# Performance work log

Measured on AMD Instinct MI355X. Metric: run time of the kernel, lower is better.

## Reference

```python
import jax, jax.numpy as jnp
import numpy as np

F = 4        # number of factors
M = 256      # codebook size per factor
D = 8192     # hypervector dimension
B = 256      # batch of composite vectors to factorize
ITERS = 10   # resonator iterations


def setup_inputs() -> dict:
    key = jax.random.key(0)
    k1, k2 = jax.random.split(key, 2)
    # bipolar (+1/-1) codebooks, shape [F, M, D]
    cb = jnp.sign(jax.random.normal(k1, (F, M, D), dtype=jnp.float32))
    codebooks = jnp.where(cb == 0, 1.0, cb)
    # composite inputs: bind (elementwise product) of one random codevector per factor
    idx = jax.random.randint(k2, (B, F), 0, M)                       # [B, F]
    chosen = codebooks[jnp.arange(F)[None, :], idx]                  # [B, F, D]
    inp = jnp.prod(chosen, axis=1)                                   # [B, D]
    return {"input": inp, "codebooks": codebooks}


def _stage_concurrent(inp, est, codebooks):
    # est: [B, F, D]; codebooks: [F, M, D]; inp: [B, D]
    n = est.shape[1]
    # inv_others[:, f] = prod_{j != f} est[:, j]  (bipolar inverse == identity)
    inv_others = jnp.stack(
        [jnp.prod(jnp.concatenate([est[:, :f], est[:, f + 1:]], axis=1), axis=1)
         for f in range(n)], axis=1)                                  # [B, F, D]
    new_est = inp[:, None, :] * inv_others                            # bind -> [B, F, D]
    sim = jnp.einsum('bfd,fmd->bfm', new_est, codebooks)              # similarity
    # activation == 'NONE'
    out = jnp.einsum('bfm,fmd->bfd', sim, codebooks)                  # dot_similarity
    return jnp.sign(out)


def reference(input, codebooks):
    Bn = input.shape[0]
    # init estimates = multiset (sum) of each codebook, broadcast over batch
    init = jnp.broadcast_to(jnp.sum(codebooks, axis=1)[None], (Bn, F, D)).astype(input.dtype)

    def cond(state):
        _, k, done = state
        return jnp.logical_and(k < ITERS, jnp.logical_not(done))

    def body(state):
        est, k, _ = state
        new = _stage_concurrent(input, est, codebooks)
        return (new, k + 1, jnp.all(new == est))

    est, k, _ = jax.lax.while_loop(cond, body, (init, jnp.int32(0), jnp.array(False)))
    # cleanup: nearest codevector per factor (argmax similarity)
    sim = jnp.einsum('bfd,fmd->bfm', est, codebooks)
    outcome = jnp.argmax(sim, axis=-1)                                # [B, F] indices
    return outcome, k
```

## Files before the change

kernel.cpp:

```cpp
#include <hip/hip_runtime.h>

#define B_SZ 256
#define F_SZ 4
#define M_SZ 256
#define D_SZ 8192
#define NITER 10

typedef signed char i8;
typedef unsigned long long u64;
typedef signed char c16 __attribute__((ext_vector_type(16)));
typedef int v4i __attribute__((ext_vector_type(4)));

#define NBFM (B_SZ * F_SZ * M_SZ)

#define OFF_CB    ((size_t)0)
#define OFF_CBT   ((size_t)8  << 20)
#define OFF_IN8   ((size_t)16 << 20)
#define OFF_CBBT  ((size_t)18 << 20)
#define OFF_INB   ((size_t)19 << 20)
#define OFF_ESB   ((size_t)20 << 20)
#define OFF_EZB   ((size_t)21 << 20)
#define OFF_SIMX  ((size_t)22 << 20)
#define OFF_P1    ((size_t)23 << 20)
#define OFF_S32   ((size_t)48 << 20)
#define OFF_PDIG  (OFF_S32 + (size_t)F_SZ * D_SZ * 4)
#define OFF_CHG   (OFF_PDIG + (size_t)3 * F_SZ * D_SZ)


__global__ __launch_bounds__(256) void k_cvt_cb(const float* __restrict__ src,
                                                i8* __restrict__ cb, i8* __restrict__ cbt) {
  __shared__ i8 tile[32][33];
  const int bid = blockIdx.x;
  const int f = bid >> 11;
  const int rem = bid & 2047;
  const int m0 = (rem >> 8) << 5;
  const int d0 = (rem & 255) << 5;
  const int t = threadIdx.x;
  const int i = t >> 3, j = (t & 7) << 2;
  const float4 v = *(const float4*)(src + ((size_t)(f * M_SZ + m0 + i)) * D_SZ + d0 + j);
  char4 c;
  c.x = v.x > 0.f ? 1 : -1;
  c.y = v.y > 0.f ? 1 : -1;
  c.z = v.z > 0.f ? 1 : -1;
  c.w = v.w > 0.f ? 1 : -1;
  *(char4*)(cb + ((size_t)(f * M_SZ + m0 + i)) * D_SZ + d0 + j) = c;
  tile[i][j + 0] = c.x; tile[i][j + 1] = c.y; tile[i][j + 2] = c.z; tile[i][j + 3] = c.w;
  __syncthreads();
  const int dd = t >> 3, jm = (t & 7) << 2;
  char4 o;
  o.x = tile[jm + 0][dd]; o.y = tile[jm + 1][dd]; o.z = tile[jm + 2][dd]; o.w = tile[jm + 3][dd];
  *(char4*)(cbt + ((size_t)(f * D_SZ + d0 + dd)) * M_SZ + m0 + jm) = o;
}

__global__ __launch_bounds__(256) void k_cvt_in(const float* __restrict__ src, i8* __restrict__ dst) {
  const int idx = blockIdx.x * 256 + threadIdx.x;
  const float4 v = ((const float4*)src)[idx];
  char4 c;
  c.x = v.x > 0.f ? 1 : -1;
  c.y = v.y > 0.f ? 1 : -1;
  c.z = v.z > 0.f ? 1 : -1;
  c.w = v.w > 0.f ? 1 : -1;
  ((char4*)dst)[idx] = c;
}

__global__ __launch_bounds__(256) void k_pack_cb(const i8* __restrict__ cb, u64* __restrict__ cbbT) {
  const int id = blockIdx.x * 256 + threadIdx.x;
  const int f = id >> 15;
  const int rem = id & 32767;
  const int w = rem >> 8;
  const int m = rem & 255;
  const i8* src = cb + ((size_t)(f * M_SZ + m)) * D_SZ + w * 64;
  u64 r = 0;
  #pragma unroll
  for (int k = 0; k < 4; ++k) {
    c16 v = *(const c16*)(src + k * 16);
    u64 part = 0;
    #pragma unroll
    for (int j = 0; j < 16; ++j) part |= ((u64)(((unsigned char)v[j]) >> 7)) << j;
    r |= part << (k * 16);
  }
  cbbT[((size_t)(f * 128 + w)) * 256 + m] = r;
}

__global__ __launch_bounds__(256) void k_pack_in(const i8* __restrict__ in8, u64* __restrict__ inb) {
  const int id = blockIdx.x * 256 + threadIdx.x;
  const int b = id >> 7;
  const int w = id & 127;
  const i8* src = in8 + (size_t)b * D_SZ + w * 64;
  u64 r = 0;
  #pragma unroll
  for (int k = 0; k < 4; ++k) {
    c16 v = *(const c16*)(src + k * 16);
    u64 part = 0;
    #pragma unroll
    for (int j = 0; j < 16; ++j) part |= ((u64)(((unsigned char)v[j]) >> 7)) << j;
    r |= part << (k * 16);
  }
  inb[(size_t)b * 128 + w] = r;
}

__global__ __launch_bounds__(256) void k_S(const i8* __restrict__ cb, int* __restrict__ S) {
  const int id = blockIdx.x * 256 + threadIdx.x;
  const int f = id >> 13, d = id & 8191;
  const i8* p = cb + (size_t)f * M_SZ * D_SZ + d;
  int s = 0;
  for (int m = 0; m < M_SZ; ++m) s += p[(size_t)m * D_SZ];
  S[id] = s;
}

__global__ __launch_bounds__(256) void k_P(const int* __restrict__ S, i8* __restrict__ pdig) {
  const int d = blockIdx.x * 256 + threadIdx.x;
  const int s0 = S[d], s1 = S[D_SZ + d], s2 = S[2 * D_SZ + d], s3 = S[3 * D_SZ + d];
  int P[4];
  P[0] = s1 * s2 * s3;
  P[1] = s0 * s2 * s3;
  P[2] = s0 * s1 * s3;
  P[3] = s0 * s1 * s2;
  for (int f = 0; f < 4; ++f) {
    int x = P[f] >> 3;
    #pragma unroll
    for (int p = 0; p < 2; ++p) {
      const int y = x + 127;
      const int q = (y >= 0) ? (y / 255) : -((-y + 254) / 255);
      const int dg = x - q * 255;
      pdig[((size_t)(p * F_SZ + f)) * D_SZ + d] = (i8)dg;
      x = q;
    }
    pdig[((size_t)(2 * F_SZ + f)) * D_SZ + d] = (i8)x;
  }
}


__global__ __launch_bounds__(256) void ga2_kernel(
    const i8* __restrict__ in8, const i8* __restrict__ cb,
    const i8* __restrict__ pdig, int* __restrict__ p1)
{
  __shared__ __align__(16) i8 lA[64 * 48];
  __shared__ __align__(16) i8 lB[128 * 48];

  const int bid = blockIdx.x;
  const int s = bid & 7;
  const int r = bid >> 3;
  const int p = r % 3;
  const int q = r / 3;
  const int f = q & 3;
  const int ct = q >> 2;
  const int b0 = (ct >> 1) * 64;
  const int m0 = (ct & 1) * 128;
  const int ksteps = 32;
  const int kbase = s << 10;

  const int t = threadIdx.x;
  const int lane = t & 63;
  const int wv = t >> 6;
  const int wrow = (wv >> 1) * 32;
  const int wcol = (wv & 1) * 64;

  const int arow = t >> 1;
  const int aoff = (t & 1) * 16;
  const i8* pB  = cb   + ((size_t)(f * M_SZ + m0 + arow)) * D_SZ + aoff;
  const i8* pDg = pdig + ((size_t)(p * F_SZ + f)) * D_SZ + aoff;
  const i8* pIn = in8  + (size_t)(b0 + arow) * D_SZ + aoff;

  v4i acc[2][4];
  #pragma unroll
  for (int tr = 0; tr < 2; ++tr)
    #pragma unroll
    for (int tc = 0; tc < 4; ++tc) acc[tr][tc] = 0;

  c16 va = 0, vb = 0;
  {
    const int kk = kbase;
    vb = (*(const c16*)(pB + kk)) * (*(const c16*)(pDg + kk));
    if (t < 128) va = *(const c16*)(pIn + kk);
  }

  for (int j = 0; j < ksteps; ++j) {
    c16 sa = va, sb = vb;
    if (j + 1 < ksteps) {
      const int kk = kbase + (j + 1) * 32;
      vb = (*(const c16*)(pB + kk)) * (*(const c16*)(pDg + kk));
      if (t < 128) va = *(const c16*)(pIn + kk);
    }
    __syncthreads();
    if (t < 128) *(c16*)&lA[arow * 48 + aoff] = sa;
    *(c16*)&lB[arow * 48 + aoff] = sb;
    __syncthreads();

    const int rsel = lane & 15;
    const int kq = (lane >> 4) * 8;
    long af[2], bf[4];
    #pragma unroll
    for (int tr = 0; tr < 2; ++tr) af[tr] = *(const long*)&lA[(wrow + tr * 16 + rsel) * 48 + kq];
    #pragma unroll
    for (int tc = 0; tc < 4; ++tc) bf[tc] = *(const long*)&lB[(wcol + tc * 16 + rsel) * 48 + kq];
    #pragma unroll
    for (int tr = 0; tr < 2; ++tr)
      #pragma unroll
      for (int tc = 0; tc < 4; ++tc)
        acc[tr][tc] = __builtin_amdgcn_mfma_i32_16x16x32_i8(af[tr], bf[tc], acc[tr][tc], 0, 0, 0);
  }

  const int colb = lane & 15;
  const int rowq = (lane >> 4) * 4;
  const size_t obase = (size_t)(p * 8 + s) * NBFM;
  #pragma unroll
  for (int tr = 0; tr < 2; ++tr)
    #pragma unroll
    for (int tc = 0; tc < 4; ++tc)
      #pragma unroll
      for (int rr = 0; rr < 4; ++rr) {
        const int b = b0 + wrow + tr * 16 + rowq + rr;
        const int m = m0 + wcol + tc * 16 + colb;
        p1[obase + (((size_t)(b * F_SZ + f)) << 8) + m] = acc[tr][tc][rr];
      }
}

__global__ __launch_bounds__(256) void k_digits1(const int* __restrict__ p1, i8* __restrict__ simx) {
  const int idx = blockIdx.x * 256 + threadIdx.x;
  long long g[3];
  #pragma unroll
  for (int p = 0; p < 3; ++p) {
    long long gg = 0;
    #pragma unroll
    for (int s = 0; s < 8; ++s) gg += (long long)p1[(size_t)(p * 8 + s) * NBFM + idx];
    g[p] = gg;
  }
  const long long sim = g[0] + 255LL * g[1] + 65025LL * g[2];
  int x = (int)sim;
  const int r1 = (x + 128) >> 8;
  const int d0 = x - (r1 << 8);
  const int r2 = (r1 + 128) >> 8;
  const int d1 = r1 - (r2 << 8);
  const size_t bf = (size_t)(idx >> 8);
  const int m = idx & 255;
  simx[bf * 768 + m] = (i8)d0;
  simx[bf * 768 + 256 + m] = (i8)d1;
  simx[bf * 768 + 512 + m] = (i8)r2;
}


__global__ __launch_bounds__(256) void ga_bit(
    const u64* __restrict__ esb, const u64* __restrict__ ezb,
    const u64* __restrict__ inb, const u64* __restrict__ cbbT,
    i8* __restrict__ simx, const int* __restrict__ changed, int it)
{
  __shared__ u64 AL[128][4];
  __shared__ int C0[2];

  if (changed[it - 1] == 0) return;

  const int bid = blockIdx.x;
  const int f = bid & 3;
  const int b0 = (bid >> 2) * 2;
  const int t = threadIdx.x;
  if (t < 2) C0[t] = 0;
  __syncthreads();

  {
    const int r = t >> 7, w = t & 127;
    const int b = b0 + r;
    int ffs[3]; int c = 0;
    for (int ff = 0; ff < 4; ++ff) if (ff != f) ffs[c++] = ff;
    const size_t base = (size_t)b * 4 * 128;
    const u64 s = inb[(size_t)b * 128 + w]
      ^ esb[base + ffs[0] * 128 + w] ^ esb[base + ffs[1] * 128 + w] ^ esb[base + ffs[2] * 128 + w];
    const u64 nz = ~(ezb[base + ffs[0] * 128 + w] | ezb[base + ffs[1] * 128 + w] | ezb[base + ffs[2] * 128 + w]);
    AL[w][r * 2] = s;
    AL[w][r * 2 + 1] = nz;
    int pcv = (int)__popcll(nz);
    #pragma unroll
    for (int off = 32; off >= 1; off >>= 1) pcv += __shfl_down(pcv, off);
    if ((t & 63) == 0) atomicAdd(&C0[r], pcv);
  }
  __syncthreads();

  const int m = t;
  int a0 = 0, a1 = 0;
  const u64* pc = cbbT + (size_t)f * 128 * 256 + m;
  #pragma unroll 4
  for (int w = 0; w < 128; ++w) {
    const u64 cbw = pc[w * 256];
    const u64 s0 = AL[w][0], z0 = AL[w][1], s1 = AL[w][2], z1 = AL[w][3];
    a0 += (int)__popcll((s0 ^ cbw) & z0);
    a1 += (int)__popcll((s1 ^ cbw) & z1);
  }
  const int sim0 = C0[0] - 2 * a0;
  const int sim1 = C0[1] - 2 * a1;

  int d1 = (sim0 + 128) >> 8; int d0v = sim0 - (d1 << 8);
  const size_t bf0 = ((size_t)b0 * 4 + f) * 768;
  simx[bf0 + m] = (i8)d0v; simx[bf0 + 256 + m] = (i8)d1;
  d1 = (sim1 + 128) >> 8; d0v = sim1 - (d1 << 8);
  const size_t bf1 = ((size_t)(b0 + 1) * 4 + f) * 768;
  simx[bf1 + m] = (i8)d0v; simx[bf1 + 256 + m] = (i8)d1;
}


template<int NP, bool FIRST>
__global__ __launch_bounds__(256) void gb_kernel(
    const i8* __restrict__ simx, const i8* __restrict__ cbt,
    u64* __restrict__ esb, u64* __restrict__ ezb,
    const int* __restrict__ S32,
    int* __restrict__ changed, int it)
{
  __shared__ __align__(16) i8 lB[8 * 8 * 64 * 8];
  __shared__ int chgf;

  if (!FIRST) { if (changed[it - 1] == 0) return; }

  const int bid = blockIdx.x;
  const int f = bid & 3;
  const int ct = bid >> 2;
  const int b0 = (ct >> 6) * 64;
  const int d0 = (ct & 63) * 128;

  const int t = threadIdx.x;
  if (t == 0) chgf = 0;
  const int lane = t & 63;
  const int wv = t >> 6;
  const int wrow = (wv >> 1) * 32;
  const int wcol = (wv & 1) * 64;

  {
    const int c = t & 15;
    const int dr0 = t >> 4;
    const int ks = c >> 1;
    const int q0 = (c & 1) * 2;
    #pragma unroll
    for (int i = 0; i < 8; ++i) {
      const int dr = dr0 + i * 16;
      union { c16 v; u64 u[2]; } x;
      x.v = *(const c16*)(cbt + ((size_t)(f * D_SZ + d0 + dr)) * M_SZ + c * 16);
      const int tile = dr >> 4;
      const int col = dr & 15;
      *(u64*)&lB[((((ks * 8 + tile) * 4 + q0) * 16 + col)) * 8] = x.u[0];
      *(u64*)&lB[((((ks * 8 + tile) * 4 + q0 + 1) * 16 + col)) * 8] = x.u[1];
    }
  }
  __syncthreads();

  v4i acc[NP][2][4];
  #pragma unroll
  for (int pp = 0; pp < NP; ++pp)
    #pragma unroll
    for (int tr = 0; tr < 2; ++tr)
      #pragma unroll
      for (int tc = 0; tc < 4; ++tc) acc[pp][tr][tc] = 0;

  const int rsel = lane & 15;
  const int kq = (lane >> 4) * 8;
  const int tb = wcol >> 4;

  #pragma unroll
  for (int ks = 0; ks < 8; ++ks) {
    long bf[4];
    #pragma unroll
    for (int tc = 0; tc < 4; ++tc)
      bf[tc] = *(const long*)&lB[((ks * 8 + tb + tc) * 64 + lane) * 8];
    #pragma unroll
    for (int pp = 0; pp < NP; ++pp) {
      long af[2];
      #pragma unroll
      for (int tr = 0; tr < 2; ++tr) {
        const int row = b0 + wrow + tr * 16 + rsel;
        af[tr] = *(const long*)(simx + ((size_t)(row * 4 + f)) * 768 + pp * 256 + ks * 32 + kq);
      }
      #pragma unroll
      for (int tr = 0; tr < 2; ++tr)
        #pragma unroll
        for (int tc = 0; tc < 4; ++tc)
          acc[pp][tr][tc] = __builtin_amdgcn_mfma_i32_16x16x32_i8(af[tr], bf[tc], acc[pp][tr][tc], 0, 0, 0);
    }
  }

  bool chl = false;
  const int colb = lane & 15;

  #pragma unroll
  for (int tr = 0; tr < 2; ++tr) {
    unsigned long long bs[4][4], bz[4][4];
    #pragma unroll
    for (int rr = 0; rr < 4; ++rr)
      #pragma unroll
      for (int tc = 0; tc < 4; ++tc) {
        int o = acc[0][tr][tc][rr];
        if (NP > 1) o += acc[1][tr][tc][rr] * 256;
        if (NP > 2) o += acc[2][tr][tc][rr] * 65536;
        bs[rr][tc] = __ballot(o < 0);
        bz[rr][tc] = __ballot(o == 0);
        if (FIRST) {
          const int sg = (o > 0) - (o < 0);
          const int d = d0 + wcol + tc * 16 + colb;
          chl |= (sg != S32[f * D_SZ + d]);
        }
      }
    u64 ws = 0, wz = 0;
    #pragma unroll
    for (int rl = 0; rl < 16; ++rl) {
      const int g = rl >> 2, rr = rl & 3;
      u64 vs = 0, vz = 0;
      #pragma unroll
      for (int tc = 0; tc < 4; ++tc) {
        vs |= ((bs[rr][tc] >> (g * 16)) & 0xFFFFull) << (tc * 16);
        vz |= ((bz[rr][tc] >> (g * 16)) & 0xFFFFull) << (tc * 16);
      }
      if (lane == rl) { ws = vs; wz = vz; }
    }
    if (lane < 16) {
      const int row = b0 + wrow + tr * 16 + lane;
      const size_t wi = ((size_t)(row * 4 + f)) * 128 + ((d0 + wcol) >> 6);
      if (!FIRST) chl |= (ws != esb[wi]) | (wz != ezb[wi]);
      esb[wi] = ws;
      ezb[wi] = wz;
    }
  }
  if (chl) atomicOr(&chgf, 1);
  __syncthreads();
  if (t == 0 && chgf) atomicOr(&changed[it], 1);
}


__global__ __launch_bounds__(256) void k_final(
    const u64* __restrict__ esb, const u64* __restrict__ ezb,
    const u64* __restrict__ cbbT, const int* __restrict__ chg,
    int* __restrict__ out)
{
  __shared__ u64 AL[128][4];
  __shared__ int C0[2];
  __shared__ long long red0[256], red1[256];

  const int bid = blockIdx.x;
  const int f = bid & 3;
  const int b0 = (bid >> 2) * 2;
  const int t = threadIdx.x;
  if (t < 2) C0[t] = 0;
  __syncthreads();

  {
    const int r = t >> 7, w = t & 127;
    const int b = b0 + r;
    const size_t a = ((size_t)b * 4 + f) * 128 + w;
    const u64 s = esb[a];
    const u64 nz = ~ezb[a];
    AL[w][r * 2] = s;
    AL[w][r * 2 + 1] = nz;
    int pcv = (int)__popcll(nz);
    #pragma unroll
    for (int off = 32; off >= 1; off >>= 1) pcv += __shfl_down(pcv, off);
    if ((t & 63) == 0) atomicAdd(&C0[r], pcv);
  }
  __syncthreads();

  const int m = t;
  int a0 = 0, a1 = 0;
  const u64* pc = cbbT + (size_t)f * 128 * 256 + m;
  #pragma unroll 4
  for (int w = 0; w < 128; ++w) {
    const u64 cbw = pc[w * 256];
    const u64 s0 = AL[w][0], z0 = AL[w][1], s1 = AL[w][2], z1 = AL[w][3];
    a0 += (int)__popcll((s0 ^ cbw) & z0);
    a1 += (int)__popcll((s1 ^ cbw) & z1);
  }
  const int sim0 = C0[0] - 2 * a0;
  const int sim1 = C0[1] - 2 * a1;

  red0[m] = ((long long)sim0 << 32) | (long long)(unsigned)(255 - m);
  red1[m] = ((long long)sim1 << 32) | (long long)(unsigned)(255 - m);
  __syncthreads();
  for (int s2 = 128; s2 > 0; s2 >>= 1) {
    if (m < s2) {
      if (red0[m + s2] > red0[m]) red0[m] = red0[m + s2];
      if (red1[m + s2] > red1[m]) red1[m] = red1[m + s2];
    }
    __syncthreads();
  }
  if (m == 0) {
    out[b0 * 4 + f] = 255 - (int)(red0[0] & 0xFFFF);
    out[(b0 + 1) * 4 + f] = 255 - (int)(red1[0] & 0xFFFF);
    if (bid == 0) {
      int k = NITER;
      for (int i = 1; i <= NITER; ++i) if (chg[i] == 0) { k = i; break; }
      out[B_SZ * F_SZ] = k;
    }
  }
}


extern "C" void kernel_launch(void* const* d_in, const int* in_sizes, int n_in,
                              void* d_out, int out_size, void* d_ws, size_t ws_size,
                              hipStream_t stream) {
  const float* f_in = (const float*)d_in[0];
  const float* f_cb = (const float*)d_in[1];
  int* out = (int*)d_out;
  char* ws = (char*)d_ws;

  i8*  cb8  = (i8*)(ws + OFF_CB);
  i8*  cbt8 = (i8*)(ws + OFF_CBT);
  i8*  in8  = (i8*)(ws + OFF_IN8);
  u64* cbbT = (u64*)(ws + OFF_CBBT);
  u64* inb  = (u64*)(ws + OFF_INB);
  u64* esb  = (u64*)(ws + OFF_ESB);
  u64* ezb  = (u64*)(ws + OFF_EZB);
  i8*  simx = (i8*)(ws + OFF_SIMX);
  int* p1   = (int*)(ws + OFF_P1);
  int* S32  = (int*)(ws + OFF_S32);
  i8*  pdig = (i8*)(ws + OFF_PDIG);
  int* chg  = (int*)(ws + OFF_CHG);

  hipMemsetAsync(chg, 0, 64, stream);
  k_cvt_cb<<<dim3(8192), dim3(256), 0, stream>>>(f_cb, cb8, cbt8);
  k_cvt_in<<<dim3(2048), dim3(256), 0, stream>>>(f_in, in8);
  k_pack_cb<<<dim3(512), dim3(256), 0, stream>>>(cb8, cbbT);
  k_pack_in<<<dim3(128), dim3(256), 0, stream>>>(in8, inb);
  k_S<<<dim3(128), dim3(256), 0, stream>>>(cb8, S32);
  k_P<<<dim3(32), dim3(256), 0, stream>>>(S32, pdig);

  ga2_kernel<<<dim3(768), dim3(256), 0, stream>>>(in8, cb8, pdig, p1);
  k_digits1<<<dim3(1024), dim3(256), 0, stream>>>(p1, simx);
  gb_kernel<3, true><<<dim3(1024), dim3(256), 0, stream>>>(
      simx, cbt8, esb, ezb, S32, chg, 1);

  for (int it = 2; it <= NITER; ++it) {
    ga_bit<<<dim3(512), dim3(256), 0, stream>>>(esb, ezb, inb, cbbT, simx, chg, it);
    gb_kernel<2, false><<<dim3(1024), dim3(256), 0, stream>>>(
        simx, cbt8, esb, ezb, nullptr, chg, it);
  }

  k_final<<<dim3(512), dim3(256), 0, stream>>>(esb, ezb, cbbT, chg, out);
}
```

Before: 564.2 us.

## Stage A-operand in LDS with swizzled B tile, split popcount kernels to 512 threads

gb_kernel now copies each block's 64-row slice of simx into padded shared memory once, so MFMA A fragments come from LDS instead of strided global loads. It also XOR-swizzles the B tile in LDS to cut bank conflicts. ga_bit and k_final go from 256 to 512 threads, with each thread handling one batch row instead of two, which raises parallelism in the popcount loops. The cost is more LDS per block in gb_kernel, which may lower occupancy, and only half the threads do the bit-packing prologue.

```diff
diff --git a/kernel.cpp b/kernel.cpp
--- a/kernel.cpp
+++ b/kernel.cpp
@@ -240,7 +240,7 @@
 }
 
 
-__global__ __launch_bounds__(256) void ga_bit(
+__global__ __launch_bounds__(512) void ga_bit(
     const u64* __restrict__ esb, const u64* __restrict__ ezb,
     const u64* __restrict__ inb, const u64* __restrict__ cbbT,
     i8* __restrict__ simx, const int* __restrict__ changed, int it)
@@ -257,7 +257,7 @@
   if (t < 2) C0[t] = 0;
   __syncthreads();
 
-  {
+  if (t < 256) {
     const int r = t >> 7, w = t & 127;
     const int b = b0 + r;
     int ffs[3]; int c = 0;
@@ -275,25 +275,22 @@
   }
   __syncthreads();
 
-  const int m = t;
-  int a0 = 0, a1 = 0;
+  const int r = t >> 8;
+  const int m = t & 255;
+  int a = 0;
   const u64* pc = cbbT + (size_t)f * 128 * 256 + m;
-  #pragma unroll 4
+  #pragma unroll 8
   for (int w = 0; w < 128; ++w) {
     const u64 cbw = pc[w * 256];
-    const u64 s0 = AL[w][0], z0 = AL[w][1], s1 = AL[w][2], z1 = AL[w][3];
-    a0 += (int)__popcll((s0 ^ cbw) & z0);
-    a1 += (int)__popcll((s1 ^ cbw) & z1);
-  }
-  const int sim0 = C0[0] - 2 * a0;
-  const int sim1 = C0[1] - 2 * a1;
-
-  int d1 = (sim0 + 128) >> 8; int d0v = sim0 - (d1 << 8);
-  const size_t bf0 = ((size_t)b0 * 4 + f) * 768;
-  simx[bf0 + m] = (i8)d0v; simx[bf0 + 256 + m] = (i8)d1;
-  d1 = (sim1 + 128) >> 8; d0v = sim1 - (d1 << 8);
-  const size_t bf1 = ((size_t)(b0 + 1) * 4 + f) * 768;
-  simx[bf1 + m] = (i8)d0v; simx[bf1 + 256 + m] = (i8)d1;
+    a += (int)__popcll((AL[w][r * 2] ^ cbw) & AL[w][r * 2 + 1]);
+  }
+  const int sim = C0[r] - 2 * a;
+
+  const int d1 = (sim + 128) >> 8;
+  const int d0v = sim - (d1 << 8);
+  const size_t bf0 = ((size_t)(b0 + r) * 4 + f) * 768;
+  simx[bf0 + m] = (i8)d0v;
+  simx[bf0 + 256 + m] = (i8)d1;
 }
 
 
@@ -304,7 +301,9 @@
     const int* __restrict__ S32,
     int* __restrict__ changed, int it)
 {
+  constexpr int LASTR = NP * 256 + 8;
   __shared__ __align__(16) i8 lB[8 * 8 * 64 * 8];
+  __shared__ __align__(16) i8 lA[64 * LASTR];
   __shared__ int chgf;
 
   if (!FIRST) { if (changed[it - 1] == 0) return; }
@@ -323,10 +322,24 @@
   const int wcol = (wv & 1) * 64;
 
   {
+    constexpr int CPR = NP * 16;
+    #pragma unroll
+    for (int idx = 0; idx < 64 * CPR; idx += 256) {
+      const int id = idx + t;
+      const int row = id / CPR;
+      const int c = id - row * CPR;
+      union { c16 v; u64 u[2]; } x;
+      x.v = *(const c16*)(simx + ((size_t)((b0 + row) * 4 + f)) * 768 + c * 16);
+      *(u64*)&lA[row * LASTR + c * 16] = x.u[0];
+      *(u64*)&lA[row * LASTR + c * 16 + 8] = x.u[1];
+    }
+  }
+  {
     const int c = t & 15;
     const int dr0 = t >> 4;
     const int ks = c >> 1;
     const int q0 = (c & 1) * 2;
+    const int swz = ((ks << 1) | (q0 >> 1)) << 3;
     #pragma unroll
     for (int i = 0; i < 8; ++i) {
       const int dr = dr0 + i * 16;
@@ -334,8 +347,8 @@
       x.v = *(const c16*)(cbt + ((size_t)(f * D_SZ + d0 + dr)) * M_SZ + c * 16);
       const int tile = dr >> 4;
       const int col = dr & 15;
-      *(u64*)&lB[((((ks * 8 + tile) * 4 + q0) * 16 + col)) * 8] = x.u[0];
-      *(u64*)&lB[((((ks * 8 + tile) * 4 + q0 + 1) * 16 + col)) * 8] = x.u[1];
+      *(u64*)&lB[(((((ks * 8 + tile) * 4 + q0) * 16 + col)) * 8) ^ swz] = x.u[0];
+      *(u64*)&lB[(((((ks * 8 + tile) * 4 + q0 + 1) * 16 + col)) * 8) ^ swz] = x.u[1];
     }
   }
   __syncthreads();
@@ -354,24 +367,24 @@
 
   #pragma unroll
   for (int ks = 0; ks < 8; ++ks) {
+    const int rswz = ((ks << 1) | (lane >> 5)) << 3;
     long bf[4];
     #pragma unroll
     for (int tc = 0; tc < 4; ++tc)
-      bf[tc] = *(const long*)&lB[((ks * 8 + tb + tc) * 64 + lane) * 8];
-    #pragma unroll
-    for (int pp = 0; pp < NP; ++pp) {
-      long af[2];
-      #pragma unroll
-      for (int tr = 0; tr < 2; ++tr) {
-        const int row = b0 + wrow + tr * 16 + rsel;
-        af[tr] = *(const long*)(simx + ((size_t)(row * 4 + f)) * 768 + pp * 256 + ks * 32 + kq);
-      }
+      bf[tc] = *(const long*)&lB[((((ks * 8 + tb + tc) * 64 + lane)) * 8) ^ rswz];
+    long af[NP][2];
+    #pragma unroll
+    for (int pp = 0; pp < NP; ++pp)
+      #pragma unroll
+      for (int tr = 0; tr < 2; ++tr)
+        af[pp][tr] = *(const long*)&lA[(wrow + tr * 16 + rsel) * LASTR + pp * 256 + ks * 32 + kq];
+    #pragma unroll
+    for (int pp = 0; pp < NP; ++pp)
       #pragma unroll
       for (int tr = 0; tr < 2; ++tr)
         #pragma unroll
         for (int tc = 0; tc < 4; ++tc)
-          acc[pp][tr][tc] = __builtin_amdgcn_mfma_i32_16x16x32_i8(af[tr], bf[tc], acc[pp][tr][tc], 0, 0, 0);
-    }
+          acc[pp][tr][tc] = __builtin_amdgcn_mfma_i32_16x16x32_i8(af[pp][tr], bf[tc], acc[pp][tr][tc], 0, 0, 0);
   }
 
   bool chl = false;
@@ -421,14 +434,14 @@
 }
 
 
-__global__ __launch_bounds__(256) void k_final(
+__global__ __launch_bounds__(512) void k_final(
     const u64* __restrict__ esb, const u64* __restrict__ ezb,
     const u64* __restrict__ cbbT, const int* __restrict__ chg,
     int* __restrict__ out)
 {
   __shared__ u64 AL[128][4];
   __shared__ int C0[2];
-  __shared__ long long red0[256], red1[256];
+  __shared__ long long red[2][256];
 
   const int bid = blockIdx.x;
   const int f = bid & 3;
@@ -437,7 +450,7 @@
   if (t < 2) C0[t] = 0;
   __syncthreads();
 
-  {
+  if (t < 256) {
     const int r = t >> 7, w = t & 127;
     const int b = b0 + r;
     const size_t a = ((size_t)b * 4 + f) * 128 + w;
@@ -452,33 +465,28 @@
   }
   __syncthreads();
 
-  const int m = t;
-  int a0 = 0, a1 = 0;
+  const int r = t >> 8;
+  const int m = t & 255;
+  int a = 0;
   const u64* pc = cbbT + (size_t)f * 128 * 256 + m;
-  #pragma unroll 4
+  #pragma unroll 8
   for (int w = 0; w < 128; ++w) {
     const u64 cbw = pc[w * 256];
-    const u64 s0 = AL[w][0], z0 = AL[w][1], s1 = AL[w][2], z1 = AL[w][3];
-    a0 += (int)__popcll((s0 ^ cbw) & z0);
-    a1 += (int)__popcll((s1 ^ cbw) & z1);
-  }
-  const int sim0 = C0[0] - 2 * a0;
-  const int sim1 = C0[1] - 2 * a1;
-
-  red0[m] = ((long long)sim0 << 32) | (long long)(unsigned)(255 - m);
-  red1[m] = ((long long)sim1 << 32) | (long long)(unsigned)(255 - m);
+    a += (int)__popcll((AL[w][r * 2] ^ cbw) & AL[w][r * 2 + 1]);
+  }
+  const int sim = C0[r] - 2 * a;
+
+  red[r][m] = ((long long)sim << 32) | (long long)(unsigned)(255 - m);
   __syncthreads();
   for (int s2 = 128; s2 > 0; s2 >>= 1) {
     if (m < s2) {
-      if (red0[m + s2] > red0[m]) red0[m] = red0[m + s2];
-      if (red1[m + s2] > red1[m]) red1[m] = red1[m + s2];
+      if (red[r][m + s2] > red[r][m]) red[r][m] = red[r][m + s2];
     }
     __syncthreads();
   }
   if (m == 0) {
-    out[b0 * 4 + f] = 255 - (int)(red0[0] & 0xFFFF);
-    out[(b0 + 1) * 4 + f] = 255 - (int)(red1[0] & 0xFFFF);
-    if (bid == 0) {
+    out[(b0 + r) * 4 + f] = 255 - (int)(red[r][0] & 0xFFFF);
+    if (t == 0 && bid == 0) {
       int k = NITER;
       for (int i = 1; i <= NITER; ++i) if (chg[i] == 0) { k = i; break; }
       out[B_SZ * F_SZ] = k;
@@ -522,10 +530,10 @@
       simx, cbt8, esb, ezb, S32, chg, 1);
 
   for (int it = 2; it <= NITER; ++it) {
-    ga_bit<<<dim3(512), dim3(256), 0, stream>>>(esb, ezb, inb, cbbT, simx, chg, it);
+    ga_bit<<<dim3(512), dim3(512), 0, stream>>>(esb, ezb, inb, cbbT, simx, chg, it);
     gb_kernel<2, false><<<dim3(1024), dim3(256), 0, stream>>>(
         simx, cbt8, esb, ezb, nullptr, chg, it);
   }
 
-  k_final<<<dim3(512), dim3(256), 0, stream>>>(esb, ezb, cbbT, chg, out);
-}
+  k_final<<<dim3(512), dim3(512), 0, stream>>>(esb, ezb, cbbT, chg, out);
+}
```

Measured after the change: 538.2 us. 4.6% less time.
